# Kernel tuning notes

Hardware: AMD Instinct MI355X
Metric: run time of the kernel (lower is better)

Reference implementation:

```python
import jax, jax.numpy as jnp
import numpy as np
import math

D_MODEL = 1024
N_HEAD = 16
D_HEAD = D_MODEL // N_HEAD
SCALE = math.sqrt(D_HEAD)
B, S = 8, 512


def setup_inputs() -> dict:
    key = jax.random.key(0)
    ks = jax.random.split(key, 7)
    x = jax.random.normal(ks[0], (B, S, D_MODEL), dtype=jnp.float32)
    mask = jnp.ones((B, S), dtype=jnp.int32)
    qmask = jax.random.randint(ks[1], (B, S), 0, 2).astype(jnp.int32)
    # params
    Wqkv = jax.random.normal(ks[2], (4 * D_MODEL, D_MODEL), dtype=jnp.float32) / math.sqrt(D_MODEL)
    fc_w = jax.random.normal(ks[3], (D_MODEL, D_MODEL), dtype=jnp.float32) / math.sqrt(D_MODEL)
    fc_b = jnp.zeros((D_MODEL,), dtype=jnp.float32)
    shift = jnp.abs(jax.random.normal(ks[4], (1,), dtype=jnp.float32)) + 0.001
    bias = -jnp.abs(jax.random.normal(ks[5], (1,), dtype=jnp.float32))
    return {"x": x, "mask": mask, "qmask": qmask, "Wqkv": Wqkv,
            "fc_w": fc_w, "fc_b": fc_b, "shift": shift, "bias": bias}


def reference(x, mask, qmask, Wqkv, fc_w, fc_b, shift, bias):
    Bsz, L, D = x.shape
    qkv = x @ Wqkv.T  # [B,S,4D], no bias
    q, k1, k2, v = jnp.split(qkv, 4, axis=-1)

    def heads(t):  # [B,S,D] -> [B,H,S,dh]
        return t.reshape(Bsz, L, N_HEAD, D_HEAD).transpose(0, 2, 1, 3)

    q, k1, k2, v = heads(q), heads(k1), heads(k2), heads(v)

    attn_self = jnp.einsum('bhqd,bhkd->bhqk', q, k1)
    attn_others = jnp.einsum('bhqd,bhkd->bhqk', q, k2)
    same_spk = (qmask[:, :, None] == qmask[:, None, :])[:, None]  # [B,1,S,S]
    attn = jnp.where(same_spk, attn_self, attn_others) / SCALE

    # key padding mask
    attn = jnp.where((mask == 0)[:, None, None, :], -jnp.inf, attn)

    # Gaussian distance bias: -(shift*(i-j)^2 + bias)
    pos = jnp.arange(L, dtype=jnp.float32)
    sq_dist = (pos[:, None] - pos[None, :]) ** 2  # [S,S]
    attn = attn - (shift[0] * sq_dist + bias[0])

    p = jax.nn.softmax(attn, axis=-1)  # dropout=0 (eval)
    out = jnp.einsum('bhqk,bhkd->bhqd', p, v)
    out = out.transpose(0, 2, 1, 3).reshape(Bsz, L, D)
    return out @ fc_w.T + fc_b
```

## Files before the change

### kernel.cpp

```cpp
#include <hip/hip_runtime.h>

typedef unsigned short u16;
typedef __bf16 bf16_t;
typedef bf16_t bf16x8 __attribute__((ext_vector_type(8)));
typedef float f32x4 __attribute__((ext_vector_type(4)));
typedef u16 u16x8 __attribute__((ext_vector_type(8)));
typedef u16 u16x4 __attribute__((ext_vector_type(4)));

__device__ __forceinline__ u16 f2b(float f) {
    unsigned int u = __float_as_uint(f);
    u += 0x7fffu + ((u >> 16) & 1u);
    return (u16)(u >> 16);
}

__device__ __forceinline__ f32x4 mfma16(u16x8 a, u16x8 b, f32x4 c) {
    return __builtin_amdgcn_mfma_f32_16x16x32_bf16(
        __builtin_bit_cast(bf16x8, a), __builtin_bit_cast(bf16x8, b), c, 0, 0, 0);
}

#define GLDS16(gp, lp)                                                          \
    __builtin_amdgcn_global_load_lds(                                           \
        (const __attribute__((address_space(1))) void*)(gp),                    \
        (__attribute__((address_space(3))) void*)(lp), 16, 0, 0)

__global__ __launch_bounds__(256) void cvt3_kernel(const float* __restrict__ s0,
                                                   const float* __restrict__ s1,
                                                   const float* __restrict__ s2,
                                                   u16* __restrict__ d0,
                                                   u16* __restrict__ d1,
                                                   u16* __restrict__ d2) {
    int i = (blockIdx.x * 256 + threadIdx.x) * 4;
    const float* src; u16* dst;
    if (i < 4194304)       { src = s0;           dst = d0;           }
    else if (i < 8388608)  { src = s1 - 4194304; dst = d1 - 4194304; }
    else                   { src = s2 - 8388608; dst = d2 - 8388608; }
    float4 f = *(const float4*)(src + i);
    u16x4 o = { f2b(f.x), f2b(f.y), f2b(f.z), f2b(f.w) };
    *(u16x4*)(dst + i) = o;
}

__global__ __launch_bounds__(512, 2) void gemm256_qkv(
    const u16* __restrict__ A, const u16* __restrict__ Bw,
    u16* __restrict__ Qf, u16* __restrict__ K1f,
    u16* __restrict__ K2f, u16* __restrict__ Vf)
{
    __shared__ u16 lds[4][2][8192];

    const int t = threadIdx.x;
    const int lane = t & 63;
    const int w = t >> 6;
    const int wm = w >> 2, wn = w & 3;
    const int lr = lane & 15, quad = lane >> 4;

    const int lin = blockIdx.x;
    const int swz = (lin & 7) * 32 + (lin >> 3);
    const int bx = swz & 15, by = swz >> 4;
    const int tileM = by * 256, tileN = bx * 256;

    const int srow = t >> 2;
    const int scol = ((t & 3) ^ ((t >> 3) & 3)) * 8;
    const u16* Asrc0 = A + (size_t)(tileM + srow) * 1024 + scol;
    const u16* Asrc1 = Asrc0 + (size_t)128 * 1024;
    const u16* Bsrc0 = Bw + (size_t)(tileN + srow) * 1024 + scol;
    const u16* Bsrc1 = Bsrc0 + (size_t)128 * 1024;

    const int swzq = (quad ^ ((lr >> 1) & 3)) * 8;
    const int aoff = (wm * 128 + lr) * 32 + swzq;
    const int boff = (wn * 64 + lr) * 32 + swzq;

    f32x4 acc[8][4] = {};

#define STAGE_A(tk, buf)                                                        \
    do { GLDS16(Asrc0 + (tk) * 32, &lds[buf][0][t * 8]);                        \
         GLDS16(Asrc1 + (tk) * 32, &lds[buf][0][(t + 512) * 8]); } while (0)
#define STAGE_B(tk, buf)                                                        \
    do { GLDS16(Bsrc0 + (tk) * 32, &lds[buf][1][t * 8]);                        \
         GLDS16(Bsrc1 + (tk) * 32, &lds[buf][1][(t + 512) * 8]); } while (0)

#define DO_TILE(tk, DO_ST, VMASM)                                               \
    do {                                                                        \
        const int cur_ = (tk) & 3, nxt_ = ((tk) + 3) & 3;                       \
        const u16* aL = &lds[cur_][0][0];                                       \
        const u16* bL = &lds[cur_][1][0];                                       \
        if (DO_ST) { STAGE_A((tk) + 3, nxt_); STAGE_B((tk) + 3, nxt_); }        \
        u16x8 af[8], bf[4];                                                     \
        _Pragma("unroll") for (int i = 0; i < 4; ++i)                           \
            bf[i] = *(const u16x8*)(bL + boff + i * 512);                       \
        _Pragma("unroll") for (int i = 0; i < 8; ++i)                           \
            af[i] = *(const u16x8*)(aL + aoff + i * 512);                       \
        __builtin_amdgcn_s_setprio(1);                                          \
        _Pragma("unroll") for (int mi = 0; mi < 8; ++mi)                        \
            _Pragma("unroll") for (int ni = 0; ni < 4; ++ni)                    \
                acc[mi][ni] = mfma16(af[mi], bf[ni], acc[mi][ni]);              \
        __builtin_amdgcn_s_setprio(0);                                          \
        VMASM;                                                                  \
        __builtin_amdgcn_s_barrier();                                           \
    } while (0)

    STAGE_A(0, 0); STAGE_B(0, 0);
    STAGE_A(1, 1); STAGE_B(1, 1);
    STAGE_A(2, 2); STAGE_B(2, 2);
    asm volatile("s_waitcnt vmcnt(8)" ::: "memory");
    __builtin_amdgcn_s_barrier();

#pragma unroll 4
    for (int tk = 0; tk < 28; ++tk)
        DO_TILE(tk, true, asm volatile("s_waitcnt vmcnt(8)" ::: "memory"));
    DO_TILE(28, true,  asm volatile("s_waitcnt vmcnt(8)" ::: "memory"));
    DO_TILE(29, false, asm volatile("s_waitcnt vmcnt(4)" ::: "memory"));
    DO_TILE(30, false, asm volatile("s_waitcnt vmcnt(0)" ::: "memory"));
    DO_TILE(31, false, (void)0);
#undef DO_TILE
#undef STAGE_A
#undef STAGE_B

    const int kv = tileN >> 10;
    const int h  = ((tileN + wn * 64) >> 6) & 15;
    const int bh = (((tileM + wm * 128) >> 9) << 4) + h;
    const int M16 = ((tileM & 511) + wm * 128) >> 4;
    const int M32 = M16 >> 1;

    if (kv < 3) {
        u16* base = (kv == 0) ? Qf : (kv == 1) ? K1f : K2f;
#pragma unroll
        for (int mi = 0; mi < 8; ++mi)
#pragma unroll
            for (int ni = 0; ni < 4; ++ni) {
                size_t idx0 = ((size_t)((bh * 32 + M16 + mi) * 2 + (ni >> 1))) * 512
                            + (((ni * 2 + (lr >> 3)) & 3) * 16 + quad * 4) * 8 + (lr & 7);
#pragma unroll
                for (int r = 0; r < 4; ++r)
                    base[idx0 + r * 8] = f2b(acc[mi][ni][r]);
            }
    } else {
#pragma unroll
        for (int mi = 0; mi < 8; ++mi)
#pragma unroll
            for (int ni = 0; ni < 4; ++ni) {
                size_t idx = ((size_t)((bh * 4 + ni) * 16 + M32 + (mi >> 1))) * 512
                           + (((mi * 2 + (quad >> 1)) & 3) * 16 + lr) * 8 + (quad & 1) * 4;
                u16x4 o = { f2b(acc[mi][ni][0]), f2b(acc[mi][ni][1]),
                            f2b(acc[mi][ni][2]), f2b(acc[mi][ni][3]) };
                *(u16x4*)(Vf + idx) = o;
            }
    }
}

template <int MT, int MODE>
__global__ __launch_bounds__(256) void gemm_bt(
    const u16* __restrict__ A, const u16* __restrict__ Bw,
    u16* __restrict__ Qf, u16* __restrict__ K1f,
    u16* __restrict__ K2f, u16* __restrict__ Vf,
    float* __restrict__ Cf, const float* __restrict__ biasp)
{
    constexpr int K = 1024;
    constexpr int MF = MT / 32;
    __shared__ u16 As[2][MT * 32];
    __shared__ u16 Bs[2][128 * 32];
    const int t = threadIdx.x;
    const int lane = t & 63;
    const int w = t >> 6;
    const int wm = w >> 1, wn = w & 1;
    const int lr = lane & 15, quad = lane >> 4;
    const int tileM = blockIdx.y * MT, tileN = blockIdx.x * 128;

    f32x4 acc[MF][4] = {};

    const u16* Ag = A + (size_t)(tileM + (t >> 2)) * K + (t & 3) * 8;
    const u16* Bg = Bw + (size_t)(tileN + (t >> 2)) * K + (t & 3) * 8;

#define STAGE(kk, bufi)                                                         \
    do {                                                                        \
        GLDS16(Ag + (kk), &As[bufi][t * 8]);                                    \
        if (MT == 128) GLDS16(Ag + (kk) + 64 * K, &As[bufi][t * 8 + 2048]);     \
        GLDS16(Bg + (kk), &Bs[bufi][t * 8]);                                    \
        GLDS16(Bg + (kk) + 64 * K, &Bs[bufi][t * 8 + 2048]);                    \
    } while (0)

    STAGE(0, 0);
    __syncthreads();

#pragma unroll 2
    for (int kk = 0; kk < K; kk += 32) {
        const int cur = (kk >> 5) & 1;
        if (kk + 32 < K) STAGE(kk + 32, cur ^ 1);

        u16x8 af[MF], bf[4];
#pragma unroll
        for (int i = 0; i < MF; ++i)
            af[i] = *(const u16x8*)(&As[cur][(wm * (MT / 2) + i * 16 + lr) * 32 + quad * 8]);
#pragma unroll
        for (int i = 0; i < 4; ++i)
            bf[i] = *(const u16x8*)(&Bs[cur][(wn * 64 + i * 16 + lr) * 32 + quad * 8]);
#pragma unroll
        for (int mi = 0; mi < MF; ++mi)
#pragma unroll
            for (int ni = 0; ni < 4; ++ni)
                acc[mi][ni] = mfma16(af[mi], bf[ni], acc[mi][ni]);

        __syncthreads();
    }
#undef STAGE

    if (MODE == 0) {
#pragma unroll
        for (int mi = 0; mi < MF; ++mi)
#pragma unroll
            for (int ni = 0; ni < 4; ++ni) {
                int n = tileN + wn * 64 + ni * 16 + lr;
                int kv = n >> 10;
                int h = (n >> 6) & 15, d = n & 63;
#pragma unroll
                for (int r = 0; r < 4; ++r) {
                    int m = tileM + wm * (MT / 2) + mi * 16 + quad * 4 + r;
                    int s = m & 511, bh = ((m >> 9) << 4) + h;
                    u16 v = f2b(acc[mi][ni][r]);
                    if (kv < 3) {
                        u16* base = (kv == 0) ? Qf : (kv == 1) ? K1f : K2f;
                        size_t idx = ((size_t)((bh * 32 + (s >> 4)) * 2 + (d >> 5))) * 512
                                   + (((d >> 3) & 3) * 16 + (s & 15)) * 8 + (d & 7);
                        base[idx] = v;
                    } else {
                        size_t idx = ((size_t)((bh * 4 + (d >> 4)) * 16 + (s >> 5))) * 512
                                   + (((s >> 3) & 3) * 16 + (d & 15)) * 8 + (s & 7);
                        Vf[idx] = v;
                    }
                }
            }
    } else {
#pragma unroll
        for (int mi = 0; mi < MF; ++mi)
#pragma unroll
            for (int ni = 0; ni < 4; ++ni) {
                int n = tileN + wn * 64 + ni * 16 + lr;
                float bv = biasp[n];
#pragma unroll
                for (int r = 0; r < 4; ++r) {
                    int m = tileM + wm * (MT / 2) + mi * 16 + quad * 4 + r;
                    Cf[(size_t)m * 1024 + n] = acc[mi][ni][r] + bv;
                }
            }
    }
}

__global__ __launch_bounds__(256) void attn_kernel(
    const u16* __restrict__ qfm, const u16* __restrict__ k1fm,
    const u16* __restrict__ k2fm, const u16* __restrict__ vfm,
    const int* __restrict__ maskp, const int* __restrict__ qmaskp,
    const float* __restrict__ shiftp, const float* __restrict__ biasp,
    u16* __restrict__ ao)
{
    __shared__ u16 Ks[2][2][2][2][512];
    __shared__ u16 Vs[2][4][512];
    __shared__ u16 Pw[4][512];

    const int bh = blockIdx.x & 127, qt = blockIdx.x >> 7;
    const int b = bh >> 4;
    const int t = threadIdx.x, lane = t & 63, w = t >> 6;
    const int lr = lane & 15, quad = lane >> 4;
    const float shiftv = shiftp[0], biasv = biasp[0];

    const int m16 = qt * 4 + w;
    const int qbase = m16 * 16;

    const u16* qsrc = qfm + ((size_t)(bh * 32 + m16) * 2) * 512 + lane * 8;
    u16x8 qa0 = *(const u16x8*)(qsrc);
    u16x8 qa1 = *(const u16x8*)(qsrc + 512);

    int qmr[4]; float rowf[4];
#pragma unroll
    for (int r = 0; r < 4; ++r) {
        int m = qbase + quad * 4 + r;
        qmr[r] = qmaskp[b * 512 + m];
        rowf[r] = (float)m;
    }

    f32x4 o0 = {0.f,0.f,0.f,0.f}, o1 = {0.f,0.f,0.f,0.f};
    f32x4 o2 = {0.f,0.f,0.f,0.f}, o3 = {0.f,0.f,0.f,0.f};
    float lsum[4] = {0.f, 0.f, 0.f, 0.f};

    u16* pbuf = &Pw[w][0];
    const int wa0 = quad * 128 + (((lr >> 3) ^ quad) * 8) + (lr & 7);
    const int wa1 = quad * 128 + (((2 | (lr >> 3)) ^ quad) * 8) + (lr & 7);
    const int ra = lr * 32 + ((quad ^ (lr >> 2)) * 8);

    const int s_ = w >> 1, kh_ = w & 1;
    const u16* k1s = k1fm + ((size_t)(bh * 32 + s_) * 2 + kh_) * 512 + lane * 8;
    const u16* k2s = k2fm + ((size_t)(bh * 32 + s_) * 2 + kh_) * 512 + lane * 8;
    const u16* vsrc = vfm + ((size_t)(bh * 4 + w) * 16) * 512 + lane * 8;

#define ASTAGE(cc, bufi)                                                        \
    do {                                                                        \
        GLDS16(k1s + (size_t)(cc) * 2048, &Ks[bufi][0][s_][kh_][lane * 8]);     \
        GLDS16(k2s + (size_t)(cc) * 2048, &Ks[bufi][1][s_][kh_][lane * 8]);     \
        GLDS16(vsrc + (size_t)(cc) * 512, &Vs[bufi][w][lane * 8]);              \
    } while (0)

    const int* qmb = qmaskp + b * 512;
    const int* kmb = maskp + b * 512;

    ASTAGE(0, 0);
    __syncthreads();

    for (int cc = 0; cc < 16; ++cc) {
        const int cur = cc & 1;
        if (cc < 15) ASTAGE(cc + 1, cur ^ 1);

        u16x8 k1t0a = *(const u16x8*)(&Ks[cur][0][0][0][lane * 8]);
        u16x8 k1t0b = *(const u16x8*)(&Ks[cur][0][0][1][lane * 8]);
        u16x8 k1t1a = *(const u16x8*)(&Ks[cur][0][1][0][lane * 8]);
        u16x8 k1t1b = *(const u16x8*)(&Ks[cur][0][1][1][lane * 8]);
        u16x8 k2t0a = *(const u16x8*)(&Ks[cur][1][0][0][lane * 8]);
        u16x8 k2t0b = *(const u16x8*)(&Ks[cur][1][0][1][lane * 8]);
        u16x8 k2t1a = *(const u16x8*)(&Ks[cur][1][1][0][lane * 8]);
        u16x8 k2t1b = *(const u16x8*)(&Ks[cur][1][1][1][lane * 8]);

        f32x4 z = {0.f, 0.f, 0.f, 0.f};
        f32x4 s1t0 = mfma16(qa1, k1t0b, mfma16(qa0, k1t0a, z));
        f32x4 s2t0 = mfma16(qa1, k2t0b, mfma16(qa0, k2t0a, z));
        f32x4 s1t1 = mfma16(qa1, k1t1b, mfma16(qa0, k1t1a, z));
        f32x4 s2t1 = mfma16(qa1, k2t1b, mfma16(qa0, k2t1a, z));

        const int col0 = cc * 32 + lr, col1 = col0 + 16;
        const int qmc0 = qmb[col0], qmc1 = qmb[col1];
        const float ka0 = (kmb[col0] ? 0.f : -1e30f) - 10.0f;
        const float ka1 = (kmb[col1] ? 0.f : -1e30f) - 10.0f;
        const float colf0 = (float)col0, colf1 = (float)col1;

        float p0[4], p1[4];
#pragma unroll
        for (int r = 0; r < 4; ++r) {
            float d0 = rowf[r] - colf0;
            float d1 = rowf[r] - colf1;
            float sel0 = (qmr[r] == qmc0) ? s1t0[r] : s2t0[r];
            float sel1 = (qmr[r] == qmc1) ? s1t1[r] : s2t1[r];
            float v0 = fmaf(sel0, 0.125f, -fmaf(shiftv * d0, d0, biasv)) + ka0;
            float v1 = fmaf(sel1, 0.125f, -fmaf(shiftv * d1, d1, biasv)) + ka1;
            p0[r] = __expf(v0);
            p1[r] = __expf(v1);
            lsum[r] += p0[r] + p1[r];
        }
#pragma unroll
        for (int r = 0; r < 4; ++r) {
            pbuf[wa0 + r * 32] = f2b(p0[r]);
            pbuf[wa1 + r * 32] = f2b(p1[r]);
        }
        u16x8 af = *(const u16x8*)(pbuf + ra);

        o0 = mfma16(af, *(const u16x8*)(&Vs[cur][0][lane * 8]), o0);
        o1 = mfma16(af, *(const u16x8*)(&Vs[cur][1][lane * 8]), o1);
        o2 = mfma16(af, *(const u16x8*)(&Vs[cur][2][lane * 8]), o2);
        o3 = mfma16(af, *(const u16x8*)(&Vs[cur][3][lane * 8]), o3);

        __syncthreads();
    }
#undef ASTAGE

#pragma unroll
    for (int r = 0; r < 4; ++r) {
        float s = lsum[r];
#pragma unroll
        for (int m = 1; m < 16; m <<= 1) s += __shfl_xor(s, m);
        float inv = 1.0f / s;
        int grow = b * 512 + qbase + quad * 4 + r;
        u16* orow = ao + (size_t)grow * 1024 + (bh & 15) * 64 + lr;
        orow[0]  = f2b(o0[r] * inv);
        orow[16] = f2b(o1[r] * inv);
        orow[32] = f2b(o2[r] * inv);
        orow[48] = f2b(o3[r] * inv);
    }
}

extern "C" void kernel_launch(void* const* d_in, const int* in_sizes, int n_in,
                              void* d_out, int out_size, void* d_ws, size_t ws_size,
                              hipStream_t stream) {
    (void)in_sizes; (void)n_in; (void)out_size; (void)ws_size;
    const float* x      = (const float*)d_in[0];
    const int*   maskp  = (const int*)d_in[1];
    const int*   qmaskp = (const int*)d_in[2];
    const float* Wqkv   = (const float*)d_in[3];
    const float* fc_w   = (const float*)d_in[4];
    const float* fc_b   = (const float*)d_in[5];
    const float* shiftp = (const float*)d_in[6];
    const float* biasp  = (const float*)d_in[7];
    float* out = (float*)d_out;

    char* ws = (char*)d_ws;
    u16* xb   = (u16*)(ws);
    u16* wb   = (u16*)(ws + (8u << 20));
    u16* fwb  = (u16*)(ws + (16u << 20));
    u16* qfm  = (u16*)(ws + (18u << 20));
    u16* k1fm = (u16*)(ws + (26u << 20));
    u16* k2fm = (u16*)(ws + (34u << 20));
    u16* vfm  = (u16*)(ws + (42u << 20));
    u16* aob  = (u16*)(ws + (50u << 20));

    cvt3_kernel<<<9216, 256, 0, stream>>>(x, Wqkv, fc_w, xb, wb, fwb);
    gemm256_qkv<<<256, 512, 0, stream>>>(xb, wb, qfm, k1fm, k2fm, vfm);
    attn_kernel<<<1024, 256, 0, stream>>>(qfm, k1fm, k2fm, vfm, maskp, qmaskp,
                                          shiftp, biasp, aob);
    gemm_bt<64, 1><<<dim3(8, 64), 256, 0, stream>>>(aob, fwb, nullptr, nullptr,
                                                    nullptr, nullptr, out, fc_b);
}
```

Baseline: 186.9 us.

## Process two query tiles per wave to reuse staged K/V tiles

Each wave in the attention kernel now handles two 16-row query tiles instead of one, so every K1/K2/V chunk loaded into LDS feeds twice the MFMA work. The grid halves from 1024 to 512 blocks and the P scratch buffer doubles per wave. This cuts global and LDS traffic per unit of compute. In exchange it raises register pressure and lowers parallelism, leaving fewer blocks to fill the CUs.

```diff
diff --git a/kernel.cpp b/kernel.cpp
--- a/kernel.cpp
+++ b/kernel.cpp
@@ -243,7 +243,7 @@
     }
 }
 
-__global__ __launch_bounds__(256) void attn_kernel(
+__global__ __launch_bounds__(256, 2) void attn_kernel(
     const u16* __restrict__ qfm, const u16* __restrict__ k1fm,
     const u16* __restrict__ k2fm, const u16* __restrict__ vfm,
     const int* __restrict__ maskp, const int* __restrict__ qmaskp,
@@ -252,34 +252,43 @@
 {
     __shared__ u16 Ks[2][2][2][2][512];
     __shared__ u16 Vs[2][4][512];
-    __shared__ u16 Pw[4][512];
-
-    const int bh = blockIdx.x & 127, qt = blockIdx.x >> 7;
+    __shared__ u16 Pw[4][2][512];
+
+    const int bh = blockIdx.x & 127, qh = blockIdx.x >> 7;
     const int b = bh >> 4;
     const int t = threadIdx.x, lane = t & 63, w = t >> 6;
     const int lr = lane & 15, quad = lane >> 4;
     const float shiftv = shiftp[0], biasv = biasp[0];
 
-    const int m16 = qt * 4 + w;
-    const int qbase = m16 * 16;
-
-    const u16* qsrc = qfm + ((size_t)(bh * 32 + m16) * 2) * 512 + lane * 8;
-    u16x8 qa0 = *(const u16x8*)(qsrc);
-    u16x8 qa1 = *(const u16x8*)(qsrc + 512);
-
-    int qmr[4]; float rowf[4];
+    const int m16a = qh * 8 + w;
+    const int m16b = m16a + 4;
+    const int qbaseA = m16a * 16;
+    const int qbaseB = m16b * 16;
+
+    const u16* qsrcA = qfm + ((size_t)(bh * 32 + m16a) * 2) * 512 + lane * 8;
+    const u16* qsrcB = qfm + ((size_t)(bh * 32 + m16b) * 2) * 512 + lane * 8;
+    u16x8 qa0 = *(const u16x8*)(qsrcA);
+    u16x8 qa1 = *(const u16x8*)(qsrcA + 512);
+    u16x8 qb0 = *(const u16x8*)(qsrcB);
+    u16x8 qb1 = *(const u16x8*)(qsrcB + 512);
+
+    int qmrA[4], qmrB[4]; float rowfA[4], rowfB[4];
 #pragma unroll
     for (int r = 0; r < 4; ++r) {
-        int m = qbase + quad * 4 + r;
-        qmr[r] = qmaskp[b * 512 + m];
-        rowf[r] = (float)m;
-    }
-
-    f32x4 o0 = {0.f,0.f,0.f,0.f}, o1 = {0.f,0.f,0.f,0.f};
-    f32x4 o2 = {0.f,0.f,0.f,0.f}, o3 = {0.f,0.f,0.f,0.f};
-    float lsum[4] = {0.f, 0.f, 0.f, 0.f};
-
-    u16* pbuf = &Pw[w][0];
+        int ma = qbaseA + quad * 4 + r;
+        int mb = qbaseB + quad * 4 + r;
+        qmrA[r] = qmaskp[b * 512 + ma];
+        qmrB[r] = qmaskp[b * 512 + mb];
+        rowfA[r] = (float)ma;
+        rowfB[r] = (float)mb;
+    }
+
+    f32x4 oa0 = {0,0,0,0}, oa1 = {0,0,0,0}, oa2 = {0,0,0,0}, oa3 = {0,0,0,0};
+    f32x4 ob0 = {0,0,0,0}, ob1 = {0,0,0,0}, ob2 = {0,0,0,0}, ob3 = {0,0,0,0};
+    float lsa[4] = {0,0,0,0}, lsb[4] = {0,0,0,0};
+
+    u16* pbA = &Pw[w][0][0];
+    u16* pbB = &Pw[w][1][0];
     const int wa0 = quad * 128 + (((lr >> 3) ^ quad) * 8) + (lr & 7);
     const int wa1 = quad * 128 + (((2 | (lr >> 3)) ^ quad) * 8) + (lr & 7);
     const int ra = lr * 32 + ((quad ^ (lr >> 2)) * 8);
@@ -316,10 +325,14 @@
         u16x8 k2t1b = *(const u16x8*)(&Ks[cur][1][1][1][lane * 8]);
 
         f32x4 z = {0.f, 0.f, 0.f, 0.f};
-        f32x4 s1t0 = mfma16(qa1, k1t0b, mfma16(qa0, k1t0a, z));
-        f32x4 s2t0 = mfma16(qa1, k2t0b, mfma16(qa0, k2t0a, z));
-        f32x4 s1t1 = mfma16(qa1, k1t1b, mfma16(qa0, k1t1a, z));
-        f32x4 s2t1 = mfma16(qa1, k2t1b, mfma16(qa0, k2t1a, z));
+        f32x4 sa1t0 = mfma16(qa1, k1t0b, mfma16(qa0, k1t0a, z));
+        f32x4 sa2t0 = mfma16(qa1, k2t0b, mfma16(qa0, k2t0a, z));
+        f32x4 sa1t1 = mfma16(qa1, k1t1b, mfma16(qa0, k1t1a, z));
+        f32x4 sa2t1 = mfma16(qa1, k2t1b, mfma16(qa0, k2t1a, z));
+        f32x4 sb1t0 = mfma16(qb1, k1t0b, mfma16(qb0, k1t0a, z));
+        f32x4 sb2t0 = mfma16(qb1, k2t0b, mfma16(qb0, k2t0a, z));
+        f32x4 sb1t1 = mfma16(qb1, k1t1b, mfma16(qb0, k1t1a, z));
+        f32x4 sb2t1 = mfma16(qb1, k2t1b, mfma16(qb0, k2t1a, z));
 
         const int col0 = cc * 32 + lr, col1 = col0 + 16;
         const int qmc0 = qmb[col0], qmc1 = qmb[col1];
@@ -327,30 +340,61 @@
         const float ka1 = (kmb[col1] ? 0.f : -1e30f) - 10.0f;
         const float colf0 = (float)col0, colf1 = (float)col1;
 
-        float p0[4], p1[4];
-#pragma unroll
-        for (int r = 0; r < 4; ++r) {
-            float d0 = rowf[r] - colf0;
-            float d1 = rowf[r] - colf1;
-            float sel0 = (qmr[r] == qmc0) ? s1t0[r] : s2t0[r];
-            float sel1 = (qmr[r] == qmc1) ? s1t1[r] : s2t1[r];
-            float v0 = fmaf(sel0, 0.125f, -fmaf(shiftv * d0, d0, biasv)) + ka0;
-            float v1 = fmaf(sel1, 0.125f, -fmaf(shiftv * d1, d1, biasv)) + ka1;
-            p0[r] = __expf(v0);
-            p1[r] = __expf(v1);
-            lsum[r] += p0[r] + p1[r];
+        u16x8 vf0 = *(const u16x8*)(&Vs[cur][0][lane * 8]);
+        u16x8 vf1 = *(const u16x8*)(&Vs[cur][1][lane * 8]);
+        u16x8 vf2 = *(const u16x8*)(&Vs[cur][2][lane * 8]);
+        u16x8 vf3 = *(const u16x8*)(&Vs[cur][3][lane * 8]);
+
+        {
+            float p0[4], p1[4];
+#pragma unroll
+            for (int r = 0; r < 4; ++r) {
+                float d0 = rowfA[r] - colf0;
+                float d1 = rowfA[r] - colf1;
+                float sel0 = (qmrA[r] == qmc0) ? sa1t0[r] : sa2t0[r];
+                float sel1 = (qmrA[r] == qmc1) ? sa1t1[r] : sa2t1[r];
+                float v0 = fmaf(sel0, 0.125f, -fmaf(shiftv * d0, d0, biasv)) + ka0;
+                float v1 = fmaf(sel1, 0.125f, -fmaf(shiftv * d1, d1, biasv)) + ka1;
+                p0[r] = __expf(v0);
+                p1[r] = __expf(v1);
+                lsa[r] += p0[r] + p1[r];
+            }
+#pragma unroll
+            for (int r = 0; r < 4; ++r) {
+                pbA[wa0 + r * 32] = f2b(p0[r]);
+                pbA[wa1 + r * 32] = f2b(p1[r]);
+            }
+            u16x8 af = *(const u16x8*)(pbA + ra);
+            oa0 = mfma16(af, vf0, oa0);
+            oa1 = mfma16(af, vf1, oa1);
+            oa2 = mfma16(af, vf2, oa2);
+            oa3 = mfma16(af, vf3, oa3);
         }
-#pragma unroll
-        for (int r = 0; r < 4; ++r) {
-            pbuf[wa0 + r * 32] = f2b(p0[r]);
-            pbuf[wa1 + r * 32] = f2b(p1[r]);
+        {
+            float p0[4], p1[4];
+#pragma unroll
+            for (int r = 0; r < 4; ++r) {
+                float d0 = rowfB[r] - colf0;
+                float d1 = rowfB[r] - colf1;
+                float sel0 = (qmrB[r] == qmc0) ? sb1t0[r] : sb2t0[r];
+                float sel1 = (qmrB[r] == qmc1) ? sb1t1[r] : sb2t1[r];
+                float v0 = fmaf(sel0, 0.125f, -fmaf(shiftv * d0, d0, biasv)) + ka0;
+                float v1 = fmaf(sel1, 0.125f, -fmaf(shiftv * d1, d1, biasv)) + ka1;
+                p0[r] = __expf(v0);
+                p1[r] = __expf(v1);
+                lsb[r] += p0[r] + p1[r];
+            }
+#pragma unroll
+            for (int r = 0; r < 4; ++r) {
+                pbB[wa0 + r * 32] = f2b(p0[r]);
+                pbB[wa1 + r * 32] = f2b(p1[r]);
+            }
+            u16x8 af = *(const u16x8*)(pbB + ra);
+            ob0 = mfma16(af, vf0, ob0);
+            ob1 = mfma16(af, vf1, ob1);
+            ob2 = mfma16(af, vf2, ob2);
+            ob3 = mfma16(af, vf3, ob3);
         }
-        u16x8 af = *(const u16x8*)(pbuf + ra);
-
-        o0 = mfma16(af, *(const u16x8*)(&Vs[cur][0][lane * 8]), o0);
-        o1 = mfma16(af, *(const u16x8*)(&Vs[cur][1][lane * 8]), o1);
-        o2 = mfma16(af, *(const u16x8*)(&Vs[cur][2][lane * 8]), o2);
-        o3 = mfma16(af, *(const u16x8*)(&Vs[cur][3][lane * 8]), o3);
 
         __syncthreads();
     }
@@ -358,16 +402,29 @@
 
 #pragma unroll
     for (int r = 0; r < 4; ++r) {
-        float s = lsum[r];
+        float s = lsa[r];
 #pragma unroll
         for (int m = 1; m < 16; m <<= 1) s += __shfl_xor(s, m);
         float inv = 1.0f / s;
-        int grow = b * 512 + qbase + quad * 4 + r;
+        int grow = b * 512 + qbaseA + quad * 4 + r;
         u16* orow = ao + (size_t)grow * 1024 + (bh & 15) * 64 + lr;
-        orow[0]  = f2b(o0[r] * inv);
-        orow[16] = f2b(o1[r] * inv);
-        orow[32] = f2b(o2[r] * inv);
-        orow[48] = f2b(o3[r] * inv);
+        orow[0]  = f2b(oa0[r] * inv);
+        orow[16] = f2b(oa1[r] * inv);
+        orow[32] = f2b(oa2[r] * inv);
+        orow[48] = f2b(oa3[r] * inv);
+    }
+#pragma unroll
+    for (int r = 0; r < 4; ++r) {
+        float s = lsb[r];
+#pragma unroll
+        for (int m = 1; m < 16; m <<= 1) s += __shfl_xor(s, m);
+        float inv = 1.0f / s;
+        int grow = b * 512 + qbaseB + quad * 4 + r;
+        u16* orow = ao + (size_t)grow * 1024 + (bh & 15) * 64 + lr;
+        orow[0]  = f2b(ob0[r] * inv);
+        orow[16] = f2b(ob1[r] * inv);
+        orow[32] = f2b(ob2[r] * inv);
+        orow[48] = f2b(ob3[r] * inv);
     }
 }
 
@@ -397,8 +454,8 @@
 
     cvt3_kernel<<<9216, 256, 0, stream>>>(x, Wqkv, fc_w, xb, wb, fwb);
     gemm256_qkv<<<256, 512, 0, stream>>>(xb, wb, qfm, k1fm, k2fm, vfm);
-    attn_kernel<<<1024, 256, 0, stream>>>(qfm, k1fm, k2fm, vfm, maskp, qmaskp,
-                                          shiftp, biasp, aob);
+    attn_kernel<<<512, 256, 0, stream>>>(qfm, k1fm, k2fm, vfm, maskp, qmaskp,
+                                         shiftp, biasp, aob);
     gemm_bt<64, 1><<<dim3(8, 64), 256, 0, stream>>>(aob, fwb, nullptr, nullptr,
                                                     nullptr, nullptr, out, fc_b);
 }
```

Result: no change. 185.4 us (-0.8%).
